# Optimization experiments

Measured on AMD Instinct MI355X. Metric: run time of the kernel, lower is better.

The kernel has to match this reference:

```python
import jax, jax.numpy as jnp
import numpy as np

DIM = 192
STATE = 64
B = 8
H = 64
W = 64
EPS_LN = 1e-5
EPS_BN = 1e-5


def _layernorm(x, g, b):
    m = jnp.mean(x, axis=-1, keepdims=True)
    v = jnp.mean((x - m) ** 2, axis=-1, keepdims=True)
    return (x - m) / jnp.sqrt(v + EPS_LN) * g + b


def _linear(x, w, b=None):
    # torch Linear convention: w is [out, in]
    y = jnp.einsum('...i,oi->...o', x, w)
    return y if b is None else y + b


def _parallel_scan(A, Bd, xp):
    # A, Bd, xp: [B, L, S]; h_t = A_t*h_{t-1} + Bd_t*xp_t via log-space cumsum
    A_safe = jnp.clip(A, 0.001, 0.999)
    log_A = jnp.log(A_safe + 1e-10)
    log_cum_A = jnp.cumsum(log_A, axis=1)
    log_cum_A_max = jnp.max(log_cum_A, axis=1, keepdims=True)
    cum_A = jnp.exp(log_cum_A - log_cum_A_max)
    BX = Bd * xp
    # prepend zeros, drop last: normalizer uses cumprod up to t-1
    log_pad = jnp.pad(log_cum_A - log_cum_A_max, ((0, 0), (1, 0), (0, 0)))[:, :-1]
    BX_norm = BX * jnp.exp(-log_pad)
    return jnp.cumsum(BX_norm, axis=1) * cum_A


def _ssm(x, ln_g, ln_b, xp_w, xp_b, dt_w, dt_b, A_log, B_w, C_w, Dp, out_w, out_b):
    xn = _layernorm(x, ln_g, ln_b)
    delta = jax.nn.softplus(_linear(xn, dt_w, dt_b)) * 0.01 + 0.0001  # [B,L,S]
    B_t = _linear(xn, B_w)
    C_t = _linear(xn, C_w)
    A = -jnp.exp(A_log)  # [S]
    x_proj = _linear(xn, xp_w, xp_b)
    deltaA = jnp.clip(delta * A, -10.0, -0.0001)
    A_disc = jnp.exp(deltaA)
    B_disc = delta * B_t
    h = _parallel_scan(A_disc, B_disc, x_proj)
    y = C_t * h
    y = jnp.where(jnp.all(jnp.isfinite(y)), y, jnp.zeros_like(y))
    y = _linear(y, out_w, out_b)
    return y + jnp.clip(Dp, -2.0, 2.0) * x


def reference(x, ln1_g, ln1_b, ln2_g, ln2_b, dw_w, bn_g, bn_b, bn_rm, bn_rv,
              ssm_ln_g, ssm_ln_b, xp_w, xp_b, dt_w, dt_b, A_log, B_w, C_w,
              D_param, out_w, out_b, mlp_w1, mlp_b1, mlp_w2, mlp_b2,
              alpha_local, alpha_ssm, alpha_mlp):
    identity = x
    # depthwise 3x3 conv + BatchNorm2d (eval mode, running stats)
    xc = jax.lax.conv_general_dilated(
        x, dw_w, (1, 1), 'SAME', feature_group_count=DIM,
        dimension_numbers=('NCHW', 'OIHW', 'NCHW'))
    scale = (bn_g / jnp.sqrt(bn_rv + EPS_BN))[None, :, None, None]
    x_local = (xc - bn_rm[None, :, None, None]) * scale + bn_b[None, :, None, None]
    # SSM branch on flattened spatial sequence
    x_seq = x.transpose(0, 2, 3, 1).reshape(B, H * W, DIM)
    x_seq = _layernorm(x_seq, ln1_g, ln1_b)
    x_seq = _ssm(x_seq, ssm_ln_g, ssm_ln_b, xp_w, xp_b, dt_w, dt_b, A_log,
                 B_w, C_w, D_param, out_w, out_b)
    x_ssm = x_seq.reshape(B, H, W, DIM).transpose(0, 3, 1, 2)
    xr = identity + alpha_local * x_local + alpha_ssm * x_ssm
    # residual MLP (dropout = identity at inference)
    x_mlp = xr.transpose(0, 2, 3, 1).reshape(B, H * W, DIM)
    x_mlp = _layernorm(x_mlp, ln2_g, ln2_b)
    x_mlp = _linear(jax.nn.gelu(_linear(x_mlp, mlp_w1, mlp_b1), approximate=False),
                    mlp_w2, mlp_b2)
    return xr + alpha_mlp * x_mlp.reshape(B, H, W, DIM).transpose(0, 3, 1, 2)


def setup_inputs() -> dict:
    key = jax.random.key(0)
    ks = jax.random.split(key, 12)
    def nrm(k, shape, s):
        return jax.random.normal(k, shape, jnp.float32) * s
    f32 = jnp.float32
    return {
        'x': jax.random.normal(ks[0], (B, DIM, H, W), f32),
        'ln1_g': jnp.ones(DIM, f32), 'ln1_b': jnp.zeros(DIM, f32),
        'ln2_g': jnp.ones(DIM, f32), 'ln2_b': jnp.zeros(DIM, f32),
        'dw_w': nrm(ks[1], (DIM, 1, 3, 3), 0.2),
        'bn_g': jnp.ones(DIM, f32), 'bn_b': jnp.zeros(DIM, f32),
        'bn_rm': jnp.zeros(DIM, f32), 'bn_rv': jnp.ones(DIM, f32),
        'ssm_ln_g': jnp.ones(DIM, f32), 'ssm_ln_b': jnp.zeros(DIM, f32),
        'xp_w': nrm(ks[2], (STATE, DIM), 0.05), 'xp_b': jnp.zeros(STATE, f32),
        'dt_w': nrm(ks[3], (STATE, DIM), 0.05), 'dt_b': jnp.zeros(STATE, f32),
        'A_log': jnp.log(jax.random.uniform(ks[4], (STATE,), f32) * 0.8 + 0.2),
        'B_w': nrm(ks[5], (STATE, DIM), 0.05),
        'C_w': nrm(ks[6], (STATE, DIM), 0.05),
        'D_param': jnp.zeros(DIM, f32),
        'out_w': nrm(ks[7], (DIM, STATE), 0.05), 'out_b': jnp.zeros(DIM, f32),
        'mlp_w1': nrm(ks[8], (4 * DIM, DIM), 0.03), 'mlp_b1': jnp.zeros(4 * DIM, f32),
        'mlp_w2': nrm(ks[9], (DIM, 4 * DIM), 0.03), 'mlp_b2': jnp.zeros(DIM, f32),
        'alpha_local': jnp.full((1,), 0.5, f32),
        'alpha_ssm': jnp.full((1,), 0.5, f32),
        'alpha_mlp': jnp.full((1,), 0.5, f32),
    }
```

## Files before the change

### kernel.cpp

```cpp
#include <hip/hip_runtime.h>
#include <hip/hip_bf16.h>
#include <math.h>


#define DEV static __device__ __forceinline__

constexpr int Bn = 8, Dm = 192, Ln = 4096, Sn = 64, Hd = 768;

typedef __attribute__((ext_vector_type(8))) short bf16x8;
typedef __attribute__((ext_vector_type(4))) float f32x4;

DEV short f2b(float x) {
  __hip_bfloat16 h = __float2bfloat16(x);
  return *(short*)&h;
}

DEV float b2f(short x) {
  __hip_bfloat16 h = *(__hip_bfloat16*)&x;
  return __bfloat162float(h);
}

__global__ __launch_bounds__(256) void k_weights(
    const float* __restrict__ dt_w, const float* __restrict__ B_w,
    const float* __restrict__ C_w, const float* __restrict__ xp_w,
    const float* __restrict__ out_w, const float* __restrict__ w1,
    const float* __restrict__ w2, short* __restrict__ wb) {
  for (int i = blockIdx.x * 256 + threadIdx.x; i < 89088; i += 64 * 256) {
    const float4* src;
    if (i < 3072)       src = (const float4*)dt_w + i;
    else if (i < 6144)  src = (const float4*)B_w + (i - 3072);
    else if (i < 9216)  src = (const float4*)C_w + (i - 6144);
    else if (i < 12288) src = (const float4*)xp_w + (i - 9216);
    else if (i < 15360) src = (const float4*)out_w + (i - 12288);
    else if (i < 52224) src = (const float4*)w1 + (i - 15360);
    else                src = (const float4*)w2 + (i - 52224);
    float4 v = *src;
    int o = i * 4;
    wb[o] = f2b(v.x); wb[o + 1] = f2b(v.y); wb[o + 2] = f2b(v.z); wb[o + 3] = f2b(v.w);
  }
}

__global__ __launch_bounds__(256, 3) void k_fproj(
    const float* __restrict__ x,
    const float* __restrict__ g1, const float* __restrict__ b1,
    const float* __restrict__ g2, const float* __restrict__ b2,
    short* __restrict__ xln1b,
    const short* __restrict__ wcat,
    const float* __restrict__ dt_b, const float* __restrict__ xp_b,
    const float* __restrict__ A_log, float* __restrict__ aA, unsigned* __restrict__ bxc,
    float* __restrict__ sums) {
  __shared__ __align__(16) float R1f[8320];
  __shared__ __align__(16) short R2s[128 * 72];
  short* As = (short*)R1f;
  short* Bs = R2s;
  int m0 = blockIdx.x * 64, tid = threadIdx.x;
  int b = m0 >> 12, l0 = m0 & 4095;
  {
    int pix = tid >> 2, part = tid & 3, c0 = part * 48;
    const float* xb = x + (size_t)b * Dm * Ln + l0 + pix;
    float v[48];
    float s1 = 0.f, q1 = 0.f;
#pragma unroll
    for (int j = 0; j < 48; j++) {
      float t = xb[(size_t)(c0 + j) * Ln];
      v[j] = t; s1 += t; q1 += t * t;
    }
    s1 += __shfl_xor(s1, 1); s1 += __shfl_xor(s1, 2);
    q1 += __shfl_xor(q1, 1); q1 += __shfl_xor(q1, 2);
    float m = s1 * (1.f / 192.f);
    float inv = rsqrtf(q1 * (1.f / 192.f) - m * m + 1e-5f);
    float s2 = 0.f, q2 = 0.f;
#pragma unroll
    for (int j = 0; j < 48; j++) {
      float y = (v[j] - m) * inv * g1[c0 + j] + b1[c0 + j];
      v[j] = y; s2 += y; q2 += y * y;
    }
    s2 += __shfl_xor(s2, 1); s2 += __shfl_xor(s2, 2);
    q2 += __shfl_xor(q2, 1); q2 += __shfl_xor(q2, 2);
    float m2 = s2 * (1.f / 192.f);
    float inv2 = rsqrtf(q2 * (1.f / 192.f) - m2 * m2 + 1e-5f);
    size_t base = (size_t)(m0 + pix) * Dm + c0;
#pragma unroll
    for (int j = 0; j < 48; j += 8) {
      int4 yo, no;
      short* yp = (short*)&yo; short* np = (short*)&no;
#pragma unroll
      for (int k = 0; k < 8; k++) {
        float y = v[j + k];
        yp[k] = f2b(y);
        np[k] = f2b((y - m2) * inv2 * g2[c0 + j + k] + b2[c0 + j + k]);
      }
      *(int4*)&xln1b[base + j] = yo;
      *(int4*)&As[pix * 200 + c0 + j] = no;
    }
  }
  __syncthreads();
  int lane = tid & 63, l16 = lane & 15, quad = lane >> 4, w = tid >> 6;
  f32x4 acc[16] = {};
  for (int kt = 0; kt < 3; kt++) {
    int kb = kt * 64;
#pragma unroll
    for (int nh = 0; nh < 2; nh++) {
      for (int i = tid; i < 1024; i += 256) {
        int row = i >> 3, c8 = (i & 7) * 8;
        *(float4*)&Bs[row * 72 + c8] =
            *(const float4*)&wcat[(size_t)(nh * 128 + row) * 192 + kb + c8];
      }
      __syncthreads();
#pragma unroll
      for (int ks = 0; ks < 2; ks++) {
        int ko = ks * 32 + quad * 8;
        bf16x8 a0 = *(const bf16x8*)&As[(w * 16 + l16) * 200 + kb + ko];
        bf16x8 bfr[8];
#pragma unroll
        for (int j = 0; j < 8; j++) bfr[j] = *(const bf16x8*)&Bs[(j * 16 + l16) * 72 + ko];
#pragma unroll
        for (int j = 0; j < 8; j++)
          acc[nh * 8 + j] = __builtin_amdgcn_mfma_f32_16x16x32_bf16(a0, bfr[j], acc[nh * 8 + j], 0, 0, 0);
      }
      __syncthreads();
    }
  }
  float* aAs = R1f;
  float* bxs = aAs + 64 * 65;
  float Av[4], dtbv[4], xpbv[4];
#pragma unroll
  for (int ni = 0; ni < 4; ni++) {
    int s = ni * 16 + l16;
    Av[ni] = -expf(A_log[s]); dtbv[ni] = dt_b[s]; xpbv[ni] = xp_b[s];
  }
#pragma unroll
  for (int r = 0; r < 4; r++) {
    int lm = w * 16 + quad * 4 + r;
    int m = m0 + lm;
#pragma unroll
    for (int ni = 0; ni < 4; ni++) {
      int s = ni * 16 + l16;
      float z = acc[ni][r] + dtbv[ni];
      float sp = (z > 20.f) ? z : log1pf(expf(z));
      float delta = sp * 0.01f + 0.0001f;
      float bt  = acc[ni + 4][r];
      float ct  = acc[ni + 8][r];
      float xpv = acc[ni + 12][r] + xpbv[ni];
      float dA = fminf(fmaxf(delta * Av[ni], -10.f), -0.0001f);
      float Ae = fminf(fmaxf(expf(dA), 0.001f), 0.999f) + 1e-10f;
      short bxh = f2b(delta * bt * xpv);
      aA[(size_t)m * 64 + s] = Ae;
      unsigned pk = (unsigned)(unsigned short)bxh
                  | ((unsigned)(unsigned short)f2b(ct) << 16);
      bxc[(size_t)m * 64 + s] = pk;
      aAs[lm * 65 + s] = Ae;
      bxs[lm * 65 + s] = b2f(bxh);
    }
  }
  __syncthreads();
  int s = tid & 63, seg = tid >> 6, chunk = seg >> 1, sub = seg & 1;
  bool first = ((m0 & 4095) == 0) && (chunk == 0) && (sub == 0);
  float P = 1.f, H = 0.f;
  int base = chunk * 32 + sub * 16;
#pragma unroll
  for (int j = 0; j < 16; j++) {
    float a  = aAs[(base + j) * 65 + s];
    float bx = bxs[(base + j) * 65 + s];
    if (first && j == 0) { P = a; H = bx; }
    else { P *= a; H = a * (H + bx); }
  }
  float* partP = (float*)R2s;
  float* partH = partP + 256;
  partP[seg * 64 + s] = P; partH[seg * 64 + s] = H;
  __syncthreads();
  if (tid < 128) {
    int c = tid >> 6;
    float p0 = partP[(c * 2) * 64 + s], p1 = partP[(c * 2 + 1) * 64 + s];
    float h0 = partH[(c * 2) * 64 + s], h1 = partH[(c * 2 + 1) * 64 + s];
    int ci = (m0 >> 12) * 128 + ((m0 & 4095) >> 5) + c;
    sums[(ci * 2 + 0) * 64 + s] = p0 * p1;
    sums[(ci * 2 + 1) * 64 + s] = p1 * h0 + h1;
  }
}

__global__ __launch_bounds__(256) void k_conv(
    const float* __restrict__ x, const float* __restrict__ dw,
    const float* __restrict__ bn_g, const float* __restrict__ bn_b,
    const float* __restrict__ bn_rm, const float* __restrict__ bn_rv,
    const float* __restrict__ a_loc, float* __restrict__ xr,
    const float* __restrict__ sums, float* __restrict__ carries) {
  __shared__ __align__(16) float xs[64 * 64];
  int tid = threadIdx.x;
  if (blockIdx.x == 192) {
    float* Pp = xs;
    float* Hp = xs + 256;
    int b = blockIdx.y, s = tid & 63, q = tid >> 6;
    float P = 1.f, H = 0.f;
#pragma unroll 4
    for (int j = 0; j < 32; j++) {
      int ci = b * 128 + q * 32 + j;
      float a = sums[(ci * 2 + 0) * 64 + s];
      float h = sums[(ci * 2 + 1) * 64 + s];
      P *= a; H = a * H + h;
    }
    Pp[q * 64 + s] = P; Hp[q * 64 + s] = H;
    __syncthreads();
    float cur = 0.f;
    for (int qq = 0; qq < q; qq++) cur = Pp[qq * 64 + s] * cur + Hp[qq * 64 + s];
#pragma unroll 4
    for (int j = 0; j < 32; j++) {
      int ci = b * 128 + q * 32 + j;
      carries[ci * 64 + s] = cur;
      float a = sums[(ci * 2 + 0) * 64 + s];
      float h = sums[(ci * 2 + 1) * 64 + s];
      cur = a * cur + h;
    }
    return;
  }
  int d = blockIdx.x, b = blockIdx.y;
  const float* xp = x + ((size_t)b * Dm + d) * Ln;
  for (int i = tid; i < 1024; i += 256) ((float4*)xs)[i] = ((const float4*)xp)[i];
  __syncthreads();
  float w[9];
#pragma unroll
  for (int k = 0; k < 9; k++) w[k] = dw[d * 9 + k];
  float scale = bn_g[d] * rsqrtf(bn_rv[d] + 1e-5f);
  float rm = bn_rm[d], bb = bn_b[d];
  float al = a_loc[0];
  float* xo = xr + ((size_t)b * Dm + d) * Ln;
  for (int i = tid; i < 4096; i += 256) {
    int h = i >> 6, wc = i & 63;
    float acc = 0.f;
#pragma unroll
    for (int kh = 0; kh < 3; kh++) {
      int hh = h + kh - 1;
      if (hh < 0 || hh >= 64) continue;
#pragma unroll
      for (int kw = 0; kw < 3; kw++) {
        int ww2 = wc + kw - 1;
        if (ww2 < 0 || ww2 >= 64) continue;
        acc += xs[hh * 64 + ww2] * w[kh * 3 + kw];
      }
    }
    float xl = (acc - rm) * scale + bb;
    xo[i] = xs[i] + al * xl;
  }
}

__global__ __launch_bounds__(256) void k_out(
    const float* __restrict__ aA, const unsigned* __restrict__ bxc,
    const float* __restrict__ carries,
    const short* __restrict__ owb, const float* __restrict__ out_b,
    const float* __restrict__ Dp, const short* __restrict__ xln1b,
    const float* __restrict__ a_ssm, const float* __restrict__ g2,
    const float* __restrict__ bb2,
    float* __restrict__ xr, short* __restrict__ xn2) {
  __shared__ __align__(16) float smemf[64 * 193];
  short* As = (short*)smemf;
  short* Bs = (short*)smemf + 192 * 72;
  float* tile = smemf;
  int l0g = blockIdx.x * 64, tid = threadIdx.x;
  int lane = tid & 63, l16 = lane & 15, quad = lane >> 4, wv = tid >> 6;
  for (int i = tid; i < 1536; i += 256) {
    int row = i >> 3, c8 = (i & 7) * 8;
    *(float4*)&As[row * 72 + c8] = *(const float4*)&owb[row * 64 + c8];
  }
  int bb = l0g >> 12, c0 = (l0g & 4095) >> 5;
  float xrv[3][4][4];
#pragma unroll
  for (int mi = 0; mi < 3; mi++)
#pragma unroll
    for (int r = 0; r < 4; r++) {
      int d = wv * 48 + mi * 16 + quad * 4 + r;
#pragma unroll
      for (int ni = 0; ni < 4; ni++) {
        int l = l0g + ni * 16 + l16;
        xrv[mi][r][ni] = xr[((size_t)bb * Dm + d) * Ln + (l & 4095)];
      }
    }
  if (wv < 2) {
    int c = c0 + wv, s = lane;
    float h = carries[(bb * 128 + c) * 64 + s];
    const float* ap = aA + (size_t)(l0g + wv * 32) * 64;
    const unsigned* bp = bxc + (size_t)(l0g + wv * 32) * 64;
    int t = 0;
    if (c == 0) {
      unsigned u = bp[s];
      h = b2f((short)(u & 0xFFFF));
      Bs[(wv * 32) * 72 + s] = f2b(b2f((short)(u >> 16)) * h);
      t = 1;
    }
#pragma unroll 4
    for (; t < 32; t++) {
      unsigned u = bp[t * 64 + s];
      float a = ap[t * 64 + s];
      h = a * (h + b2f((short)(u & 0xFFFF)));
      Bs[(wv * 32 + t) * 72 + s] = f2b(b2f((short)(u >> 16)) * h);
    }
  }
  __syncthreads();
  f32x4 acc[3][4] = {};
#pragma unroll
  for (int ks = 0; ks < 2; ks++) {
    int ko = ks * 32 + quad * 8;
    bf16x8 a[3], b[4];
#pragma unroll
    for (int mi = 0; mi < 3; mi++) a[mi] = *(const bf16x8*)&As[(wv * 48 + mi * 16 + l16) * 72 + ko];
#pragma unroll
    for (int ni = 0; ni < 4; ni++) b[ni] = *(const bf16x8*)&Bs[(ni * 16 + l16) * 72 + ko];
#pragma unroll
    for (int mi = 0; mi < 3; mi++)
#pragma unroll
      for (int ni = 0; ni < 4; ni++)
        acc[mi][ni] = __builtin_amdgcn_mfma_f32_16x16x32_bf16(a[mi], b[ni], acc[mi][ni], 0, 0, 0);
  }
  __syncthreads();
  float as_ = a_ssm[0];
#pragma unroll
  for (int mi = 0; mi < 3; mi++)
#pragma unroll
    for (int r = 0; r < 4; r++) {
      int d = wv * 48 + mi * 16 + quad * 4 + r;
      float ob = out_b[d];
      float dc = fminf(fmaxf(Dp[d], -2.f), 2.f);
#pragma unroll
      for (int ni = 0; ni < 4; ni++) {
        int l = l0g + ni * 16 + l16;
        float v = acc[mi][ni][r] + ob;
        if (dc != 0.f) v += dc * b2f(xln1b[(size_t)l * 192 + d]);
        size_t idx = ((size_t)bb * Dm + d) * Ln + (l & 4095);
        float nx = xrv[mi][r][ni] + as_ * v;
        xr[idx] = nx;
        tile[(l & 63) * 193 + d] = nx;
      }
    }
  __syncthreads();
  int pix = tid >> 2, part = tid & 3, c0p = part * 48;
  float vv[48];
  float s1 = 0.f, q1 = 0.f;
#pragma unroll
  for (int j = 0; j < 48; j++) {
    float t = tile[pix * 193 + c0p + j];
    vv[j] = t; s1 += t; q1 += t * t;
  }
  s1 += __shfl_xor(s1, 1); s1 += __shfl_xor(s1, 2);
  q1 += __shfl_xor(q1, 1); q1 += __shfl_xor(q1, 2);
  float m = s1 * (1.f / 192.f);
  float inv = rsqrtf(q1 * (1.f / 192.f) - m * m + 1e-5f);
  size_t obase = (size_t)(l0g + pix) * Dm + c0p;
#pragma unroll
  for (int j = 0; j < 48; j += 8) {
    int4 no; short* np = (short*)&no;
#pragma unroll
    for (int k = 0; k < 8; k++)
      np[k] = f2b((vv[j + k] - m) * inv * g2[c0p + j + k] + bb2[c0p + j + k]);
    *(int4*)&xn2[obase + j] = no;
  }
}

__global__ __launch_bounds__(256) void k_gemm1(
    const short* __restrict__ xn2, const short* __restrict__ w1b,
    const float* __restrict__ b1h, short* __restrict__ hid) {
  __shared__ __align__(16) short smem[128 * 72 + 64 * 72];
  short* As = smem;
  short* Bs = smem + 128 * 72;
  int bid = blockIdx.x;
  int xcd = bid & 7, p = bid >> 3;
  int m0 = (xcd * 32 + p / 12) * 128, n0 = (p % 12) * 64;
  int tid = threadIdx.x;
  int lane = tid & 63, l16 = lane & 15, quad = lane >> 4;
  int wm = (tid >> 6) >> 1, wn = (tid >> 6) & 1;
  f32x4 acc[4][2] = {};
  for (int kt = 0; kt < 3; kt++) {
    int kb = kt * 64;
    for (int i = tid; i < 1024; i += 256) {
      int row = i >> 3, c8 = (i & 7) * 8;
      *(float4*)&As[row * 72 + c8] = *(const float4*)&xn2[(size_t)(m0 + row) * 192 + kb + c8];
    }
    for (int i = tid; i < 512; i += 256) {
      int row = i >> 3, c8 = (i & 7) * 8;
      *(float4*)&Bs[row * 72 + c8] = *(const float4*)&w1b[(size_t)(n0 + row) * 192 + kb + c8];
    }
    __syncthreads();
#pragma unroll
    for (int ks = 0; ks < 2; ks++) {
      int ko = ks * 32 + quad * 8;
      bf16x8 a[4], b[2];
#pragma unroll
      for (int mi = 0; mi < 4; mi++) a[mi] = *(const bf16x8*)&As[(wm * 64 + mi * 16 + l16) * 72 + ko];
#pragma unroll
      for (int ni = 0; ni < 2; ni++) b[ni] = *(const bf16x8*)&Bs[(wn * 32 + ni * 16 + l16) * 72 + ko];
#pragma unroll
      for (int mi = 0; mi < 4; mi++)
#pragma unroll
        for (int ni = 0; ni < 2; ni++)
          acc[mi][ni] = __builtin_amdgcn_mfma_f32_16x16x32_bf16(a[mi], b[ni], acc[mi][ni], 0, 0, 0);
    }
    __syncthreads();
  }
  short* Cs = smem;
  float bias2[2];
#pragma unroll
  for (int ni = 0; ni < 2; ni++) bias2[ni] = b1h[n0 + wn * 32 + ni * 16 + l16];
#pragma unroll
  for (int mi = 0; mi < 4; mi++)
#pragma unroll
    for (int ni = 0; ni < 2; ni++) {
      int n = wn * 32 + ni * 16 + l16;
#pragma unroll
      for (int r = 0; r < 4; r++) {
        int m = wm * 64 + mi * 16 + quad * 4 + r;
        float v = acc[mi][ni][r] + bias2[ni];
        float w2v = v * v;
        float inner = __builtin_fmaf(0.044715f * w2v, v, v);
        float e = exp2f(2.3021183f * inner);
        float g = v - __fdividef(v, 1.f + e);
        Cs[m * 72 + n] = f2b(g);
      }
    }
  __syncthreads();
  for (int i = tid; i < 1024; i += 256) {
    int m = i >> 3, ch = i & 7;
    *(float4*)&hid[(size_t)(m0 + m) * 768 + n0 + ch * 8] = *(const float4*)&Cs[m * 72 + ch * 8];
  }
}

__global__ __launch_bounds__(256) void k_gemm2(
    const short* __restrict__ hid, const short* __restrict__ w2b,
    const float* __restrict__ b2o, const float* __restrict__ xr,
    const float* __restrict__ am, float* __restrict__ out) {
  __shared__ __align__(16) short Wt[96 * 72];
  __shared__ __align__(16) short Ht[64 * 72];
  int bid = blockIdx.x;
  int xcd = bid & 7, p = bid >> 3;
  int l0g = (xcd * 64 + (p >> 1)) * 64, d0 = (p & 1) * 96;
  int tid = threadIdx.x;
  int lane = tid & 63, l16 = lane & 15, quad = lane >> 4;
  int wm = (tid >> 6) >> 1, wn = (tid >> 6) & 1;
  float xrv[3][2][4];
#pragma unroll
  for (int mi = 0; mi < 3; mi++)
#pragma unroll
    for (int r = 0; r < 4; r++) {
      int d = d0 + wm * 48 + mi * 16 + quad * 4 + r;
#pragma unroll
      for (int ni = 0; ni < 2; ni++) {
        int lg = l0g + wn * 32 + ni * 16 + l16;
        xrv[mi][ni][r] = xr[((size_t)(lg >> 12) * Dm + d) * Ln + (lg & 4095)];
      }
    }
  f32x4 acc[3][2] = {};
  for (int kt = 0; kt < 12; kt++) {
    int kb = kt * 64;
    for (int i = tid; i < 768; i += 256) {
      int row = i >> 3, c8 = (i & 7) * 8;
      *(float4*)&Wt[row * 72 + c8] = *(const float4*)&w2b[(size_t)(d0 + row) * 768 + kb + c8];
    }
    for (int i = tid; i < 512; i += 256) {
      int row = i >> 3, c8 = (i & 7) * 8;
      *(float4*)&Ht[row * 72 + c8] = *(const float4*)&hid[(size_t)(l0g + row) * 768 + kb + c8];
    }
    __syncthreads();
#pragma unroll
    for (int ks = 0; ks < 2; ks++) {
      int ko = ks * 32 + quad * 8;
      bf16x8 a[3], b[2];
#pragma unroll
      for (int mi = 0; mi < 3; mi++) a[mi] = *(const bf16x8*)&Wt[(wm * 48 + mi * 16 + l16) * 72 + ko];
#pragma unroll
      for (int ni = 0; ni < 2; ni++) b[ni] = *(const bf16x8*)&Ht[(wn * 32 + ni * 16 + l16) * 72 + ko];
#pragma unroll
      for (int mi = 0; mi < 3; mi++)
#pragma unroll
        for (int ni = 0; ni < 2; ni++)
          acc[mi][ni] = __builtin_amdgcn_mfma_f32_16x16x32_bf16(a[mi], b[ni], acc[mi][ni], 0, 0, 0);
    }
    __syncthreads();
  }
  float alpha = am[0];
#pragma unroll
  for (int mi = 0; mi < 3; mi++)
#pragma unroll
    for (int r = 0; r < 4; r++) {
      int d = d0 + wm * 48 + mi * 16 + quad * 4 + r;
      float bias = b2o[d];
#pragma unroll
      for (int ni = 0; ni < 2; ni++) {
        int lg = l0g + wn * 32 + ni * 16 + l16;
        size_t idx = ((size_t)(lg >> 12) * Dm + d) * Ln + (lg & 4095);
        out[idx] = xrv[mi][ni][r] + alpha * (acc[mi][ni][r] + bias);
      }
    }
}

extern "C" void kernel_launch(void* const* d_in, const int* in_sizes, int n_in,
                              void* d_out, int out_size, void* d_ws, size_t ws_size,
                              hipStream_t stream) {
  (void)in_sizes; (void)n_in; (void)out_size; (void)ws_size;
  const float* x     = (const float*)d_in[0];
  const float* ln1_g = (const float*)d_in[1];
  const float* ln1_b = (const float*)d_in[2];
  const float* ln2_g = (const float*)d_in[3];
  const float* ln2_b = (const float*)d_in[4];
  const float* dw_w  = (const float*)d_in[5];
  const float* bn_g  = (const float*)d_in[6];
  const float* bn_b  = (const float*)d_in[7];
  const float* bn_rm = (const float*)d_in[8];
  const float* bn_rv = (const float*)d_in[9];
  const float* ssm_g = (const float*)d_in[10];
  const float* ssm_b = (const float*)d_in[11];
  const float* xp_w  = (const float*)d_in[12];
  const float* xp_b  = (const float*)d_in[13];
  const float* dt_w  = (const float*)d_in[14];
  const float* dt_b  = (const float*)d_in[15];
  const float* A_log = (const float*)d_in[16];
  const float* B_w   = (const float*)d_in[17];
  const float* C_w   = (const float*)d_in[18];
  const float* Dp    = (const float*)d_in[19];
  const float* out_w = (const float*)d_in[20];
  const float* out_b = (const float*)d_in[21];
  const float* w1    = (const float*)d_in[22];
  const float* b1    = (const float*)d_in[23];
  const float* w2    = (const float*)d_in[24];
  const float* b2    = (const float*)d_in[25];
  const float* a_loc = (const float*)d_in[26];
  const float* a_ssm = (const float*)d_in[27];
  const float* a_mlp = (const float*)d_in[28];

  float* ws = (float*)d_ws;
  short*    xln1b = (short*)(ws + 3145728);
  float*    aA    = ws + 6291456;
  unsigned* bxc   = (unsigned*)(ws + 8388608);
  float*    xr    = ws + 17825792;
  short*    wb    = (short*)(ws + 24117248);
  float*    sums  = ws + 24829952;
  float*    carr  = ws + 24961024;
  short*    xn2   = (short*)(ws + 25026560);
  short*    hid   = (short*)(ws + 28172288);
  short*    wcatb = wb;
  short*    owb   = wb + 49152;
  short*    w1b   = wb + 61440;
  short*    w2b   = wb + 208896;
  float*    out   = (float*)d_out;

  k_weights<<<dim3(64),     256, 0, stream>>>(dt_w, B_w, C_w, xp_w, out_w, w1, w2, wb);
  k_fproj  <<<dim3(512),    256, 0, stream>>>(x, ln1_g, ln1_b, ssm_g, ssm_b, xln1b,
                                              wcatb, dt_b, xp_b, A_log, aA, bxc, sums);
  k_conv   <<<dim3(193, 8), 256, 0, stream>>>(x, dw_w, bn_g, bn_b, bn_rm, bn_rv, a_loc, xr,
                                              sums, carr);
  k_out    <<<dim3(512),    256, 0, stream>>>(aA, bxc, carr, owb, out_b, Dp, xln1b,
                                              a_ssm, ln2_g, ln2_b, xr, xn2);
  k_gemm1  <<<dim3(3072),   256, 0, stream>>>(xn2, w1b, b1, hid);
  k_gemm2  <<<dim3(1024),   256, 0, stream>>>(hid, w2b, b2, xr, a_mlp, out);
}
```

Baseline: 258.2 us.

## Shrink MLP gemm1 tile to 64x64 and load full K into LDS at once

The first MLP GEMM now uses 64x64 output tiles instead of 128x64, doubling the grid to 6144 blocks. The whole K=192 slice of A and B is staged into shared memory in a single pass, which removes the three-step K loop and its repeated barriers. Each wave computes a 16x64 strip with 4 accumulators instead of 8. The intent is more parallelism and fewer synchronisations, at the cost of lower reuse of the weight tile, more redundant loads of weights across blocks, and a larger LDS footprint per block.

```diff
diff --git a/kernel.cpp b/kernel.cpp
--- a/kernel.cpp
+++ b/kernel.cpp
@@ -357,65 +357,51 @@
 __global__ __launch_bounds__(256) void k_gemm1(
     const short* __restrict__ xn2, const short* __restrict__ w1b,
     const float* __restrict__ b1h, short* __restrict__ hid) {
-  __shared__ __align__(16) short smem[128 * 72 + 64 * 72];
-  short* As = smem;
-  short* Bs = smem + 128 * 72;
+  __shared__ __align__(16) short As[64 * 200];
+  __shared__ __align__(16) short Bs[64 * 200];
   int bid = blockIdx.x;
   int xcd = bid & 7, p = bid >> 3;
-  int m0 = (xcd * 32 + p / 12) * 128, n0 = (p % 12) * 64;
+  int m0 = (xcd * 64 + p / 12) * 64, n0 = (p % 12) * 64;
   int tid = threadIdx.x;
-  int lane = tid & 63, l16 = lane & 15, quad = lane >> 4;
-  int wm = (tid >> 6) >> 1, wn = (tid >> 6) & 1;
-  f32x4 acc[4][2] = {};
-  for (int kt = 0; kt < 3; kt++) {
-    int kb = kt * 64;
-    for (int i = tid; i < 1024; i += 256) {
-      int row = i >> 3, c8 = (i & 7) * 8;
-      *(float4*)&As[row * 72 + c8] = *(const float4*)&xn2[(size_t)(m0 + row) * 192 + kb + c8];
-    }
-    for (int i = tid; i < 512; i += 256) {
-      int row = i >> 3, c8 = (i & 7) * 8;
-      *(float4*)&Bs[row * 72 + c8] = *(const float4*)&w1b[(size_t)(n0 + row) * 192 + kb + c8];
-    }
-    __syncthreads();
-#pragma unroll
-    for (int ks = 0; ks < 2; ks++) {
-      int ko = ks * 32 + quad * 8;
-      bf16x8 a[4], b[2];
-#pragma unroll
-      for (int mi = 0; mi < 4; mi++) a[mi] = *(const bf16x8*)&As[(wm * 64 + mi * 16 + l16) * 72 + ko];
-#pragma unroll
-      for (int ni = 0; ni < 2; ni++) b[ni] = *(const bf16x8*)&Bs[(wn * 32 + ni * 16 + l16) * 72 + ko];
-#pragma unroll
-      for (int mi = 0; mi < 4; mi++)
-#pragma unroll
-        for (int ni = 0; ni < 2; ni++)
-          acc[mi][ni] = __builtin_amdgcn_mfma_f32_16x16x32_bf16(a[mi], b[ni], acc[mi][ni], 0, 0, 0);
-    }
-    __syncthreads();
-  }
-  short* Cs = smem;
-  float bias2[2];
-#pragma unroll
-  for (int ni = 0; ni < 2; ni++) bias2[ni] = b1h[n0 + wn * 32 + ni * 16 + l16];
-#pragma unroll
-  for (int mi = 0; mi < 4; mi++)
-#pragma unroll
-    for (int ni = 0; ni < 2; ni++) {
-      int n = wn * 32 + ni * 16 + l16;
-#pragma unroll
-      for (int r = 0; r < 4; r++) {
-        int m = wm * 64 + mi * 16 + quad * 4 + r;
-        float v = acc[mi][ni][r] + bias2[ni];
-        float w2v = v * v;
-        float inner = __builtin_fmaf(0.044715f * w2v, v, v);
-        float e = exp2f(2.3021183f * inner);
-        float g = v - __fdividef(v, 1.f + e);
-        Cs[m * 72 + n] = f2b(g);
-      }
-    }
-  __syncthreads();
-  for (int i = tid; i < 1024; i += 256) {
+  int lane = tid & 63, l16 = lane & 15, quad = lane >> 4, wv = tid >> 6;
+  for (int i = tid; i < 1536; i += 256) {
+    int row = i / 24, c8 = (i % 24) * 8;
+    *(float4*)&As[row * 200 + c8] = *(const float4*)&xn2[(size_t)(m0 + row) * 192 + c8];
+    *(float4*)&Bs[row * 200 + c8] = *(const float4*)&w1b[(size_t)(n0 + row) * 192 + c8];
+  }
+  __syncthreads();
+  f32x4 acc[4] = {};
+#pragma unroll
+  for (int ks = 0; ks < 6; ks++) {
+    int ko = ks * 32 + quad * 8;
+    bf16x8 a0 = *(const bf16x8*)&As[(wv * 16 + l16) * 200 + ko];
+#pragma unroll
+    for (int ni = 0; ni < 4; ni++) {
+      bf16x8 b0 = *(const bf16x8*)&Bs[(ni * 16 + l16) * 200 + ko];
+      acc[ni] = __builtin_amdgcn_mfma_f32_16x16x32_bf16(a0, b0, acc[ni], 0, 0, 0);
+    }
+  }
+  __syncthreads();
+  short* Cs = As;
+  float bias4[4];
+#pragma unroll
+  for (int ni = 0; ni < 4; ni++) bias4[ni] = b1h[n0 + ni * 16 + l16];
+#pragma unroll
+  for (int ni = 0; ni < 4; ni++) {
+    int n = ni * 16 + l16;
+#pragma unroll
+    for (int r = 0; r < 4; r++) {
+      int m = wv * 16 + quad * 4 + r;
+      float v = acc[ni][r] + bias4[ni];
+      float w2v = v * v;
+      float inner = __builtin_fmaf(0.044715f * w2v, v, v);
+      float e = exp2f(2.3021183f * inner);
+      float g = v - __fdividef(v, 1.f + e);
+      Cs[m * 72 + n] = f2b(g);
+    }
+  }
+  __syncthreads();
+  for (int i = tid; i < 512; i += 256) {
     int m = i >> 3, ch = i & 7;
     *(float4*)&hid[(size_t)(m0 + m) * 768 + n0 + ch * 8] = *(const float4*)&Cs[m * 72 + ch * 8];
   }
@@ -546,6 +532,6 @@
                                               sums, carr);
   k_out    <<<dim3(512),    256, 0, stream>>>(aA, bxc, carr, owb, out_b, Dp, xln1b,
                                               a_ssm, ln2_g, ln2_b, xr, xn2);
-  k_gemm1  <<<dim3(3072),   256, 0, stream>>>(xn2, w1b, b1, hid);
+  k_gemm1  <<<dim3(6144),   256, 0, stream>>>(xn2, w1b, b1, hid);
   k_gemm2  <<<dim3(1024),   256, 0, stream>>>(hid, w2b, b2, xr, a_mlp, out);
 }
```

Result: no change. 263.1 us (+1.9%).
